# Kernel optimization log

Measured on AMD Instinct MI355X. Metric: run time of the kernel, lower is better.

Reference implementation:

```python
import jax, jax.numpy as jnp
import numpy as np

B, H, W = 1, 48, 160
CIN, CF, D = 1024, 64, 48  # input_features, PSM_features, depth_channel = max_disp/downsample
EPS = 1e-5


def setup_inputs() -> dict:
    key = jax.random.key(0)
    ks = jax.random.split(key, 12)
    z = lambda s: jnp.zeros(s, jnp.float32)
    o = lambda s: jnp.ones(s, jnp.float32)
    return {
        "left_features": jax.random.normal(ks[0], (B, CIN, H, W), jnp.float32),
        "right_features": jax.random.normal(ks[1], (B, CIN, H, W), jnp.float32),
        "conv1_w": jax.random.normal(ks[2], (CF, CIN), jnp.float32) * 0.03,
        "conv1_b": z((CF,)),
        "bn1_g": o((CF,)), "bn1_b": z((CF,)),
        "bn1_m": jax.random.normal(ks[3], (CF,), jnp.float32) * 0.1,
        "bn1_v": jax.random.uniform(ks[4], (CF,), jnp.float32) + 0.5,
        "c3a_w": jax.random.normal(ks[5], (CF, 2 * CF, 3, 3, 3), jnp.float32) * 0.02,
        "c3a_b": z((CF,)),
        "bn3a_g": o((CF,)), "bn3a_b": z((CF,)),
        "bn3a_m": jax.random.normal(ks[6], (CF,), jnp.float32) * 0.1,
        "bn3a_v": jax.random.uniform(ks[7], (CF,), jnp.float32) + 0.5,
        "c3b_w": jax.random.normal(ks[8], (CF, CF, 3, 3, 3), jnp.float32) * 0.02,
        "c3b_b": z((CF,)),
        "bn3b_g": o((CF,)), "bn3b_b": z((CF,)),
        "bn3b_m": jax.random.normal(ks[9], (CF,), jnp.float32) * 0.1,
        "bn3b_v": jax.random.uniform(ks[10], (CF,), jnp.float32) + 0.5,
    }


def _bn(x, g, b, m, v, nsp):
    # eval-mode batchnorm; nsp = number of trailing spatial dims
    sh = (-1,) + (1,) * nsp
    return (x - m.reshape(sh)) * (g.reshape(sh) * jax.lax.rsqrt(v.reshape(sh) + EPS)) + b.reshape(sh)


def reference(left_features, right_features, conv1_w, conv1_b, bn1_g, bn1_b, bn1_m, bn1_v,
              c3a_w, c3a_b, bn3a_g, bn3a_b, bn3a_m, bn3a_v,
              c3b_w, c3b_b, bn3b_g, bn3b_b, bn3b_m, bn3b_v):
    def down(x):
        y = jnp.einsum('oi,bihw->bohw', conv1_w, x) + conv1_b[:, None, None]
        return jax.nn.relu(_bn(y, bn1_g, bn1_b, bn1_m, bn1_v, 2))

    L = down(left_features)   # [B,CF,H,W]
    R = down(right_features)  # [B,CF,H,W]

    # Vectorized shifted cost volume (replaces the Python loop over disparities).
    # For disparity d, output width j: left -> L[...,j] if j>=d else 0; right -> R[...,j-d] if j>=d else 0.
    idx = jnp.arange(W)[None, :] - jnp.arange(D)[:, None]       # [D,W]
    mask = (idx >= 0).astype(L.dtype)                           # [D,W]
    left_vol = L[:, :, :, None, :] * mask                       # [B,CF,H,D,W]
    right_vol = R[:, :, :, jnp.clip(idx, 0, W - 1)] * mask      # [B,CF,H,D,W]
    cost = jnp.concatenate([left_vol, right_vol], axis=1)       # [B,2CF,H,D,W]
    cost = jnp.transpose(cost, (0, 1, 3, 2, 4))                 # [B,2CF,D,H,W]

    def conv3(x, wk, bias):
        y = jax.lax.conv_general_dilated(x, wk, (1, 1, 1), [(1, 1)] * 3,
                                         dimension_numbers=('NCDHW', 'OIDHW', 'NCDHW'))
        return y + bias[:, None, None, None]

    y = jax.nn.relu(_bn(conv3(cost, c3a_w, c3a_b), bn3a_g, bn3a_b, bn3a_m, bn3a_v, 3))
    y = jax.nn.relu(_bn(conv3(y, c3b_w, c3b_b), bn3b_g, bn3b_b, bn3b_m, bn3b_v, 3))
    return y.reshape(B, -1, H, W)  # [B, CF*D, H, W]
```

## Files before the change

kernel.cpp:

```cpp
#include <hip/hip_runtime.h>
#include <hip/hip_bf16.h>


#define HH   48
#define WW   160
#define DDEP 48
#define CIN  1024
#define NPX  (HH*WW)
#define KSPL 16

typedef unsigned short u16;
typedef unsigned int   u32;
typedef __attribute__((ext_vector_type(8))) short bf16x8;
typedef __attribute__((ext_vector_type(4))) float f32x4;
typedef __attribute__((ext_vector_type(4))) u32   u32x4;
typedef __attribute__((ext_vector_type(2))) u32   u32x2;

__device__ __forceinline__ u16 f2bf(float f) {
    u32 u = __builtin_bit_cast(u32, f);
    u32 r = u + 0x7FFFu + ((u >> 16) & 1u);
    return (u16)(r >> 16);
}

__global__ __launch_bounds__(256) void k_prep(
    const float* __restrict__ c3a, const float* __restrict__ c3b,
    const float* __restrict__ cb3a, const float* __restrict__ g3a,
    const float* __restrict__ b3a,  const float* __restrict__ m3a,
    const float* __restrict__ v3a,
    const float* __restrict__ cb3b, const float* __restrict__ g3b,
    const float* __restrict__ b3b,  const float* __restrict__ m3b,
    const float* __restrict__ v3b,
    u16* __restrict__ wa, u16* __restrict__ wb, float* __restrict__ bnc)
{
    int tid = blockIdx.x*256 + threadIdx.x;
    if (tid < 221184) {
        int i = tid & 127, o = (tid >> 7) & 63, tap = tid >> 13;
        wa[tid] = f2bf(c3a[(o*128 + i)*27 + tap]);
    } else {
        int t2 = tid - 221184;
        if (t2 < 110592) {
            int i = t2 & 63;
            int kw = (t2 >> 6) % 3;
            int rest = t2 / 192;
            int o = rest & 63, kdkh = rest >> 6;
            wb[t2] = f2bf(c3b[(o*64 + i)*27 + (kdkh/3)*9 + (kdkh%3)*3 + kw]);
        }
    }
    if (tid < 64) {
        float s = g3a[tid] * rsqrtf(v3a[tid] + 1e-5f);
        bnc[tid]      = s;
        bnc[64 + tid] = (cb3a[tid] - m3a[tid])*s + b3a[tid];
    } else if (tid < 128) {
        int o = tid - 64;
        float s = g3b[o] * rsqrtf(v3b[o] + 1e-5f);
        bnc[128 + o] = s;
        bnc[192 + o] = (cb3b[o] - m3b[o])*s + b3b[o];
    }
}

__global__ __launch_bounds__(256) void k_conv1(
    const float* __restrict__ left, const float* __restrict__ right,
    const float* __restrict__ w1, float* __restrict__ P)
{
    __shared__ float Ws[4096];
    const int img = blockIdx.y;
    const int s   = blockIdx.z;
    const float* x = img ? right : left;
    const int tid = threadIdx.x;
    const int px = blockIdx.x*64 + (tid & 63);
    const int o0 = (tid >> 6)*16;
    const int ibase = s*(CIN/KSPL);

    #pragma unroll
    for (int q = 0; q < 4; ++q) {
        int idx = q*256 + tid;
        int o = idx >> 4, ii = (idx & 15)*4;
        *(f32x4*)(Ws + o*64 + ii) =
            *(const f32x4*)(w1 + (size_t)o*CIN + ibase + ii);
    }
    __syncthreads();

    float acc[16];
    #pragma unroll
    for (int oo = 0; oo < 16; ++oo) acc[oo] = 0.f;

    for (int it = 0; it < CIN/KSPL; it += 4) {
        const int i = ibase + it;
        float x0 = x[(i+0)*NPX + px];
        float x1 = x[(i+1)*NPX + px];
        float x2 = x[(i+2)*NPX + px];
        float x3 = x[(i+3)*NPX + px];
        #pragma unroll
        for (int oo = 0; oo < 16; ++oo) {
            const float4 wv4 = *(const float4*)(Ws + (o0+oo)*64 + it);
            acc[oo] = fmaf(wv4.w, x3, fmaf(wv4.z, x2,
                      fmaf(wv4.y, x1, fmaf(wv4.x, x0, acc[oo]))));
        }
    }
    float* dst = P + ((size_t)(s*2 + img)*NPX + px)*64 + o0;
    #pragma unroll
    for (int q = 0; q < 4; ++q)
        *(f32x4*)(dst + q*4) = *(const f32x4*)(acc + q*4);
}

__global__ __launch_bounds__(256) void k_conv1_reduce(
    const float* __restrict__ P,
    const float* __restrict__ b1,
    const float* __restrict__ g,  const float* __restrict__ bb,
    const float* __restrict__ m,  const float* __restrict__ v,
    u16* __restrict__ LRb)
{
    const int tid = blockIdx.x*256 + threadIdx.x;
    const int f = tid*4;
    f32x4 acc = *(const f32x4*)(P + f);
    #pragma unroll
    for (int s = 1; s < KSPL; ++s)
        acc += *(const f32x4*)(P + (size_t)(s*2)*(NPX*64) + f);
    const int o0 = f & 63;
    const int px = f >> 6;
    const int img = px / NPX, pxl = px - img*NPX;
    const int h = pxl / WW, w = pxl - h*WW;
    u16 res[4];
    #pragma unroll
    for (int r = 0; r < 4; ++r) {
        int o = o0 + r;
        float sc = g[o] * rsqrtf(v[o] + 1e-5f);
        float val = (acc[r] + b1[o] - m[o])*sc + bb[o];
        res[r] = f2bf(val > 0.f ? val : 0.f);
    }
    u16* dst = LRb + (size_t)img*491520 + h*10240 + (o0 >> 3)*1280
                   + w*8 + (o0 & 7);
    *(u32x2*)dst = *(const u32x2*)res;
}

__global__ __launch_bounds__(256) void k_conv3a(
    const u16* __restrict__ LRb, const u16* __restrict__ wa,
    const float* __restrict__ bnc, u16* __restrict__ yt)
{
    __shared__ u16 sm[31744];
    u16* Lt = sm;
    u16* Rt = sm + 11520;
    u16* Aw = sm + 23040;

    const int h  = blockIdx.x;
    const int d0 = blockIdx.y*2;
    const int tid = threadIdx.x;
    const int l  = tid & 63;
    const int wv = tid >> 6;
    const int dd = wv >> 1;
    const int wbase = (wv & 1)*80;
    const int l15 = l & 15, l4 = l >> 4;
    const int wcol = wbase + l15;
    const bf16x8 bzero = {0,0,0,0,0,0,0,0};

    f32x4 acc[4][5];
    #pragma unroll
    for (int a = 0; a < 4; ++a)
        #pragma unroll
        for (int b = 0; b < 5; ++b)
            acc[a][b] = (f32x4){0.f,0.f,0.f,0.f};

    for (int kh = 0; kh < 3; ++kh) {
        int hp = h + kh - 1;
        if (hp < 0 || hp >= HH) continue;
        __syncthreads();
        {
            const u16* ls = LRb + (size_t)hp*10240;
            const u16* rs = LRb + 491520 + (size_t)hp*10240;
            #pragma unroll
            for (int gq = 0; gq < 5; ++gq) {
                int eb = (gq*256 + tid)*8;
                int c = eb / 1280, rem = eb - c*1280;
                int w = rem >> 3;
                u32x4 va = *(const u32x4*)(ls + eb);
                u32x4 vb = *(const u32x4*)(rs + eb);
                *(u32x4*)(Lt + w*72 + c*8) = va;
                *(u32x4*)(Rt + w*72 + c*8) = vb;
            }
        }
        for (int kd = 0; kd < 3; ++kd) {
            int dp = d0 + dd + kd - 1;
            bool dok = (dp >= 0) && (dp < DDEP);
            for (int kw = 0; kw < 3; ++kw) {
                __syncthreads();
                {
                    const u16* as = wa + (size_t)(kd*9 + kh*3 + kw)*8192;
                    #pragma unroll
                    for (int gq = 0; gq < 4; ++gq) {
                        int eb = (gq*256 + tid)*8;
                        int o = eb >> 7, ii = eb & 127;
                        *(u32x4*)(Aw + o*136 + ii) = *(const u32x4*)(as + eb);
                    }
                }
                __syncthreads();

                int laddr[5], raddr[5];
                bool val[5];
                #pragma unroll
                for (int nf = 0; nf < 5; ++nf) {
                    int wp = wcol + nf*16 + kw - 1;
                    bool vv = dok && (wp >= 0) && (wp < WW) && (wp >= dp);
                    val[nf]   = vv;
                    laddr[nf] = (vv ? wp : 0)*72;
                    raddr[nf] = (vv ? (wp - dp) : 0)*72;
                }
                #pragma unroll
                for (int ic = 0; ic < 4; ++ic) {
                    const int kcolA = ic*32 + 8*l4;
                    bf16x8 a0 = *(const bf16x8*)(Aw + ( 0 + l15)*136 + kcolA);
                    bf16x8 a1 = *(const bf16x8*)(Aw + (16 + l15)*136 + kcolA);
                    bf16x8 a2 = *(const bf16x8*)(Aw + (32 + l15)*136 + kcolA);
                    bf16x8 a3 = *(const bf16x8*)(Aw + (48 + l15)*136 + kcolA);
                    const int kin = (ic & 1)*32 + 8*l4;
                    #pragma unroll
                    for (int nf = 0; nf < 5; ++nf) {
                        const u16* bp = (ic < 2) ? (Lt + laddr[nf] + kin)
                                                 : (Rt + raddr[nf] + kin);
                        bf16x8 b = *(const bf16x8*)bp;
                        b = val[nf] ? b : bzero;
                        acc[0][nf] = __builtin_amdgcn_mfma_f32_16x16x32_bf16(a0, b, acc[0][nf], 0, 0, 0);
                        acc[1][nf] = __builtin_amdgcn_mfma_f32_16x16x32_bf16(a1, b, acc[1][nf], 0, 0, 0);
                        acc[2][nf] = __builtin_amdgcn_mfma_f32_16x16x32_bf16(a2, b, acc[2][nf], 0, 0, 0);
                        acc[3][nf] = __builtin_amdgcn_mfma_f32_16x16x32_bf16(a3, b, acc[3][nf], 0, 0, 0);
                    }
                }
            }
        }
    }

    __syncthreads();
    u16* eps = sm + wv*5280;
    float sc[4][4], sh[4][4];
    #pragma unroll
    for (int mf = 0; mf < 4; ++mf)
        #pragma unroll
        for (int r = 0; r < 4; ++r) {
            int o = mf*16 + 4*l4 + r;
            sc[mf][r] = bnc[o];
            sh[mf][r] = bnc[64 + o];
        }
    #pragma unroll
    for (int mf = 0; mf < 4; ++mf)
        #pragma unroll
        for (int nf = 0; nf < 5; ++nf)
            #pragma unroll
            for (int r = 0; r < 4; ++r) {
                float vv = acc[mf][nf][r]*sc[mf][r] + sh[mf][r];
                vv = vv > 0.f ? vv : 0.f;
                eps[(nf*16 + l15)*66 + mf*16 + 4*l4 + r] = f2bf(vv);
            }
    const int dy = d0 + dd;
    u16* yb2 = yt + ((size_t)(dy*HH + h))*10240;
    #pragma unroll
    for (int k = 0; k < 40; ++k) {
        int flat = k*64 + l;
        int c   = flat / 320;
        int rem = flat - c*320;
        int w   = rem >> 2;
        int pr  = (rem & 3)*2;
        u32 vv = *(const u32*)(eps + w*66 + c*8 + pr);
        *(u32*)(yb2 + (size_t)c*1280 + (wbase + w)*8 + pr) = vv;
    }
}

__global__ __launch_bounds__(256) void k_conv3b(
    const u16* __restrict__ yt, const u16* __restrict__ wb,
    const float* __restrict__ bnc, float* __restrict__ outp)
{
    __shared__ u16 A2[12800];

    const int h  = blockIdx.x;
    const int d0 = blockIdx.y*2;
    const int tid = threadIdx.x;
    const int l  = tid & 63;
    const int wv = tid >> 6;
    const int dd = wv >> 1;
    const int wbase = (wv & 1)*80;
    const int l15 = l & 15, l4 = l >> 4;
    const int wcol = wbase + l15;
    const bf16x8 bzero = {0,0,0,0,0,0,0,0};

    f32x4 acc[4][5];
    #pragma unroll
    for (int a = 0; a < 4; ++a)
        #pragma unroll
        for (int b = 0; b < 5; ++b)
            acc[a][b] = (f32x4){0.f,0.f,0.f,0.f};

    for (int kh = 0; kh < 3; ++kh) {
        int hp = h + kh - 1;
        if (hp < 0 || hp >= HH) continue;
        for (int kd = 0; kd < 3; ++kd) {
            __syncthreads();
            {
                const u16* as = wb + (size_t)(kd*3 + kh)*12288;
                #pragma unroll
                for (int q = 0; q < 6; ++q) {
                    int idx = q*256 + tid;
                    int o = idx/24;
                    int cc = (idx - o*24)*8;
                    *(u32x4*)(A2 + o*200 + cc) = *(const u32x4*)(as + (size_t)idx*8);
                }
            }
            __syncthreads();

            const int dpw = d0 + dd + kd - 1;
            const bool dok = (dpw >= 0) && (dpw < DDEP);
            const int dc = min(max(dpw, 0), DDEP-1);
            const u16* yrow = yt + ((size_t)((dc*HH + hp)*8) + l4)*1280;
            for (int kw = 0; kw < 3; ++kw) {
                int gofs[5]; bool val[5];
                #pragma unroll
                for (int nf = 0; nf < 5; ++nf) {
                    int wp = wcol + nf*16 + kw - 1;
                    bool vv = dok && (wp >= 0) && (wp < WW);
                    val[nf]  = vv;
                    gofs[nf] = (vv ? wp : 0)*8;
                }
                #pragma unroll
                for (int ic = 0; ic < 2; ++ic) {
                    const int kcolA = kw*64 + ic*32 + 8*l4;
                    bf16x8 a0 = *(const bf16x8*)(A2 + ( 0 + l15)*200 + kcolA);
                    bf16x8 a1 = *(const bf16x8*)(A2 + (16 + l15)*200 + kcolA);
                    bf16x8 a2 = *(const bf16x8*)(A2 + (32 + l15)*200 + kcolA);
                    bf16x8 a3 = *(const bf16x8*)(A2 + (48 + l15)*200 + kcolA);
                    const u16* yc = yrow + ic*5120;
                    #pragma unroll
                    for (int nf = 0; nf < 5; ++nf) {
                        bf16x8 b = *(const bf16x8*)(yc + gofs[nf]);
                        b = val[nf] ? b : bzero;
                        acc[0][nf] = __builtin_amdgcn_mfma_f32_16x16x32_bf16(a0, b, acc[0][nf], 0, 0, 0);
                        acc[1][nf] = __builtin_amdgcn_mfma_f32_16x16x32_bf16(a1, b, acc[1][nf], 0, 0, 0);
                        acc[2][nf] = __builtin_amdgcn_mfma_f32_16x16x32_bf16(a2, b, acc[2][nf], 0, 0, 0);
                        acc[3][nf] = __builtin_amdgcn_mfma_f32_16x16x32_bf16(a3, b, acc[3][nf], 0, 0, 0);
                    }
                }
            }
        }
    }

    const int dout = d0 + dd;
    #pragma unroll
    for (int mf = 0; mf < 4; ++mf)
        #pragma unroll
        for (int r = 0; r < 4; ++r) {
            int o = mf*16 + 4*l4 + r;
            float s = bnc[128 + o], t = bnc[192 + o];
            size_t base = ((size_t)(o*DDEP + dout)*HH + h)*WW + wbase;
            #pragma unroll
            for (int nf = 0; nf < 5; ++nf) {
                float vv = acc[mf][nf][r]*s + t;
                outp[base + nf*16 + l15] = vv > 0.f ? vv : 0.f;
            }
        }
}

extern "C" void kernel_launch(void* const* d_in, const int* in_sizes, int n_in,
                              void* d_out, int out_size, void* d_ws, size_t ws_size,
                              hipStream_t stream)
{
    const float* left  = (const float*)d_in[0];
    const float* right = (const float*)d_in[1];
    const float* w1    = (const float*)d_in[2];
    const float* b1    = (const float*)d_in[3];
    const float* g1    = (const float*)d_in[4];
    const float* bb1   = (const float*)d_in[5];
    const float* m1    = (const float*)d_in[6];
    const float* v1    = (const float*)d_in[7];
    const float* c3a   = (const float*)d_in[8];
    const float* cb3a  = (const float*)d_in[9];
    const float* g3a   = (const float*)d_in[10];
    const float* b3a   = (const float*)d_in[11];
    const float* m3a   = (const float*)d_in[12];
    const float* v3a   = (const float*)d_in[13];
    const float* c3b   = (const float*)d_in[14];
    const float* cb3b  = (const float*)d_in[15];
    const float* g3b   = (const float*)d_in[16];
    const float* b3b   = (const float*)d_in[17];
    const float* m3b   = (const float*)d_in[18];
    const float* v3b   = (const float*)d_in[19];

    char* ws = (char*)d_ws;
    u16*   LRb = (u16*)ws;
    u16*   wa  = (u16*)(ws + 1966080);
    u16*   wb  = (u16*)(ws + 1966080 + 442368);
    float* bnc = (float*)(ws + 1966080 + 442368 + 221184);
    u16*   yt  = (u16*)(ws + 1966080 + 442368 + 221184 + 1024);
    if (ws_size < 49816576) return;

    float* P = (float*)d_out;

    k_prep<<<dim3(1296), dim3(256), 0, stream>>>(
        c3a, c3b, cb3a, g3a, b3a, m3a, v3a, cb3b, g3b, b3b, m3b, v3b, wa, wb, bnc);
    k_conv1<<<dim3(120, 2, KSPL), dim3(256), 0, stream>>>(
        left, right, w1, P);
    k_conv1_reduce<<<dim3(960), dim3(256), 0, stream>>>(
        P, b1, g1, bb1, m1, v1, LRb);
    k_conv3a<<<dim3(48, 24), dim3(256), 0, stream>>>(LRb, wa, bnc, yt);
    k_conv3b<<<dim3(48, 24), dim3(256), 0, stream>>>(yt, wb, bnc, (float*)d_out);
}
```

Measured before the change: 320.5 us.

## Give each conv3a wave one depth slice over the full width, doubling tile reuse

Each conv3a block now covers four depth slices instead of two. Each wave owns one depth and all 160 columns (10 N-fragments), so the grid halves and every staged left/right row and weight tile is reused by twice as much work. The epilogue drops the LDS transpose and writes packed bf16 pairs straight to global memory. In exchange, accumulator registers double to 160 floats per lane, which raises register pressure; launch_bounds(256,2) is added to hold occupancy. The direct stores are also narrower and less coalesced, and fewer blocks means less parallelism across the CUs.

Result: slower. 346.7 us (+8.2%).

```diff
diff --git a/kernel.cpp b/kernel.cpp
--- a/kernel.cpp
+++ b/kernel.cpp
@@ -133,7 +133,7 @@
     *(u32x2*)dst = *(const u32x2*)res;
 }
 
-__global__ __launch_bounds__(256) void k_conv3a(
+__global__ __launch_bounds__(256, 2) void k_conv3a(
     const u16* __restrict__ LRb, const u16* __restrict__ wa,
     const float* __restrict__ bnc, u16* __restrict__ yt)
 {
@@ -143,21 +143,18 @@
     u16* Aw = sm + 23040;
 
     const int h  = blockIdx.x;
-    const int d0 = blockIdx.y*2;
+    const int d0 = blockIdx.y*4;
     const int tid = threadIdx.x;
     const int l  = tid & 63;
     const int wv = tid >> 6;
-    const int dd = wv >> 1;
-    const int wbase = (wv & 1)*80;
     const int l15 = l & 15, l4 = l >> 4;
-    const int wcol = wbase + l15;
     const bf16x8 bzero = {0,0,0,0,0,0,0,0};
 
-    f32x4 acc[4][5];
+    f32x4 acc[4][10];
     #pragma unroll
     for (int a = 0; a < 4; ++a)
         #pragma unroll
-        for (int b = 0; b < 5; ++b)
+        for (int b = 0; b < 10; ++b)
             acc[a][b] = (f32x4){0.f,0.f,0.f,0.f};
 
     for (int kh = 0; kh < 3; ++kh) {
@@ -179,7 +176,7 @@
             }
         }
         for (int kd = 0; kd < 3; ++kd) {
-            int dp = d0 + dd + kd - 1;
+            int dp = d0 + wv + kd - 1;
             bool dok = (dp >= 0) && (dp < DDEP);
             for (int kw = 0; kw < 3; ++kw) {
                 __syncthreads();
@@ -194,11 +191,11 @@
                 }
                 __syncthreads();
 
-                int laddr[5], raddr[5];
-                bool val[5];
-                #pragma unroll
-                for (int nf = 0; nf < 5; ++nf) {
-                    int wp = wcol + nf*16 + kw - 1;
+                int laddr[10], raddr[10];
+                bool val[10];
+                #pragma unroll
+                for (int nf = 0; nf < 10; ++nf) {
+                    int wp = l15 + nf*16 + kw - 1;
                     bool vv = dok && (wp >= 0) && (wp < WW) && (wp >= dp);
                     val[nf]   = vv;
                     laddr[nf] = (vv ? wp : 0)*72;
@@ -213,7 +210,7 @@
                     bf16x8 a3 = *(const bf16x8*)(Aw + (48 + l15)*136 + kcolA);
                     const int kin = (ic & 1)*32 + 8*l4;
                     #pragma unroll
-                    for (int nf = 0; nf < 5; ++nf) {
+                    for (int nf = 0; nf < 10; ++nf) {
                         const u16* bp = (ic < 2) ? (Lt + laddr[nf] + kin)
                                                  : (Rt + raddr[nf] + kin);
                         bf16x8 b = *(const bf16x8*)bp;
@@ -228,8 +225,6 @@
         }
     }
 
-    __syncthreads();
-    u16* eps = sm + wv*5280;
     float sc[4][4], sh[4][4];
     #pragma unroll
     for (int mf = 0; mf < 4; ++mf)
@@ -239,28 +234,24 @@
             sc[mf][r] = bnc[o];
             sh[mf][r] = bnc[64 + o];
         }
+    const int dy = d0 + wv;
+    u16* rowb = yt + (size_t)(dy*HH + h)*10240;
     #pragma unroll
     for (int mf = 0; mf < 4; ++mf)
         #pragma unroll
-        for (int nf = 0; nf < 5; ++nf)
+        for (int nf = 0; nf < 10; ++nf) {
+            const int w = nf*16 + l15;
             #pragma unroll
-            for (int r = 0; r < 4; ++r) {
-                float vv = acc[mf][nf][r]*sc[mf][r] + sh[mf][r];
-                vv = vv > 0.f ? vv : 0.f;
-                eps[(nf*16 + l15)*66 + mf*16 + 4*l4 + r] = f2bf(vv);
-            }
-    const int dy = d0 + dd;
-    u16* yb2 = yt + ((size_t)(dy*HH + h))*10240;
-    #pragma unroll
-    for (int k = 0; k < 40; ++k) {
-        int flat = k*64 + l;
-        int c   = flat / 320;
-        int rem = flat - c*320;
-        int w   = rem >> 2;
-        int pr  = (rem & 3)*2;
-        u32 vv = *(const u32*)(eps + w*66 + c*8 + pr);
-        *(u32*)(yb2 + (size_t)c*1280 + (wbase + w)*8 + pr) = vv;
-    }
+            for (int rp = 0; rp < 2; ++rp) {
+                int o_lo = mf*16 + 4*l4 + rp*2;
+                float v0 = acc[mf][nf][rp*2]  *sc[mf][rp*2]   + sh[mf][rp*2];
+                float v1 = acc[mf][nf][rp*2+1]*sc[mf][rp*2+1] + sh[mf][rp*2+1];
+                v0 = v0 > 0.f ? v0 : 0.f;
+                v1 = v1 > 0.f ? v1 : 0.f;
+                u32 pk = (u32)f2bf(v0) | ((u32)f2bf(v1) << 16);
+                *(u32*)(rowb + (o_lo >> 3)*1280 + w*8 + (o_lo & 7)) = pk;
+            }
+        }
 }
 
 __global__ __launch_bounds__(256) void k_conv3b(
@@ -396,6 +387,6 @@
         left, right, w1, P);
     k_conv1_reduce<<<dim3(960), dim3(256), 0, stream>>>(
         P, b1, g1, bb1, m1, v1, LRb);
-    k_conv3a<<<dim3(48, 24), dim3(256), 0, stream>>>(LRb, wa, bnc, yt);
+    k_conv3a<<<dim3(48, 12), dim3(256), 0, stream>>>(LRb, wa, bnc, yt);
     k_conv3b<<<dim3(48, 24), dim3(256), 0, stream>>>(yt, wb, bnc, (float*)d_out);
 }
```
